# Optimization experiments

Hardware: AMD Instinct MI355X
Metric: run time of the kernel (lower is better)

Reference implementation:

```python
import jax, jax.numpy as jnp
import numpy as np

N, C, D, H, W = 2, 16, 32, 128, 128
CLAMP_MIN, CLAMP_MAX = 1e-8, 1e8


def setup_inputs() -> dict:
    key = jax.random.key(0)
    k1, k2, k3 = jax.random.split(key, 3)
    pred = jax.random.uniform(k1, (N, C, D, H, W), dtype=jnp.float32)
    # target holds the discretized ordinal label, replicated across channel dim
    t = jax.random.randint(k2, (N, 1, D, H, W), 0, C, dtype=jnp.int32)
    target = jnp.broadcast_to(t, (N, C, D, H, W)).astype(jnp.int32)
    mask = jax.random.randint(k3, (N, 1, D, H, W), 0, 2, dtype=jnp.int32)
    return {"pred": pred, "target": target, "mask": mask}


def reference(pred, target, mask):
    n, c, d, h, w = pred.shape
    valid = (mask[:, 0] > 0).reshape(-1)              # [N*D*H*W]
    # channel-first flatten: matches pred.transpose(0,1) then boolean index
    p = jnp.moveaxis(pred, 1, 0).reshape(c, -1)       # [C, M]
    t = jnppos = jnp.moveaxis(target, 1, 0).reshape(c, -1)  # [C, M]
    K = jnp.arange(c, dtype=jnp.int32)[:, None]       # [C, 1]
    m0 = (K <= t) & valid[None, :]                    # ordinal bins below label
    m1 = (K > t) & valid[None, :]                     # ordinal bins above label
    log_p = jnp.log(jnp.clip(p, CLAMP_MIN, CLAMP_MAX))
    log_1mp = jnp.log(jnp.clip(1.0 - p, CLAMP_MIN, CLAMP_MAX))
    s = jnp.sum(jnp.where(m0, log_p, 0.0)) + jnp.sum(jnp.where(m1, log_1mp, 0.0))
    S = jnp.sum(valid).astype(pred.dtype)             # number of masked voxels
    return s / (-S)
```

## Files before the change

kernel.cpp:

```cpp
#include <hip/hip_runtime.h>


constexpr int  kC     = 16;
constexpr int  kDHW   = 32 * 128 * 128;
constexpr long kM     = 2L * kDHW;
constexpr int  kBlock = 256;
constexpr int  kVox   = 4;
constexpr int  kGrid  = (int)(kM / kVox / kBlock);

__global__ __launch_bounds__(kBlock)
void ordloss_main(const float* __restrict__ pred,
                  const int*   __restrict__ target,
                  const int*   __restrict__ mask,
                  float*       __restrict__ bsum,
                  int*         __restrict__ bcnt) {
    const int  tid  = blockIdx.x * kBlock + threadIdx.x;
    const long base = (long)tid * kVox;
    const int  n    = (int)(base >> 19);
    const int  sp   = (int)(base & (kDHW - 1));

    const float* pb = pred + ((size_t)n << 23) + sp;
    float4 p[kC];
    #pragma unroll
    for (int c = 0; c < kC; ++c)
        p[c] = *reinterpret_cast<const float4*>(pb + ((size_t)c << 19));
    const int4 mk = *reinterpret_cast<const int4*>(mask + base);
    const int4 tg = *reinterpret_cast<const int4*>(target + ((size_t)n << 23) + sp);

    float acc0 = 0.f, acc1 = 0.f, acc2 = 0.f, acc3 = 0.f;
    #pragma unroll
    for (int c = 0; c < kC; ++c) {
        float x0 = (c <= tg.x) ? p[c].x : 1.0f - p[c].x;
        float x1 = (c <= tg.y) ? p[c].y : 1.0f - p[c].y;
        float x2 = (c <= tg.z) ? p[c].z : 1.0f - p[c].z;
        float x3 = (c <= tg.w) ? p[c].w : 1.0f - p[c].w;
        acc0 += __logf(fmaxf(x0, 1e-8f));
        acc1 += __logf(fmaxf(x1, 1e-8f));
        acc2 += __logf(fmaxf(x2, 1e-8f));
        acc3 += __logf(fmaxf(x3, 1e-8f));
    }

    float lsum = (mk.x > 0 ? acc0 : 0.f) + (mk.y > 0 ? acc1 : 0.f)
               + (mk.z > 0 ? acc2 : 0.f) + (mk.w > 0 ? acc3 : 0.f);
    int   lcnt = (mk.x > 0) + (mk.y > 0) + (mk.z > 0) + (mk.w > 0);

    #pragma unroll
    for (int off = 32; off > 0; off >>= 1) {
        lsum += __shfl_down(lsum, off);
        lcnt += __shfl_down(lcnt, off);
    }
    __shared__ float swave[kBlock / 64];
    __shared__ int   cwave[kBlock / 64];
    const int lane = threadIdx.x & 63;
    const int wid  = threadIdx.x >> 6;
    if (lane == 0) { swave[wid] = lsum; cwave[wid] = lcnt; }
    __syncthreads();
    if (threadIdx.x == 0) {
        bsum[blockIdx.x] = swave[0] + swave[1] + swave[2] + swave[3];
        bcnt[blockIdx.x] = cwave[0] + cwave[1] + cwave[2] + cwave[3];
    }
}

__global__ __launch_bounds__(kBlock)
void ordloss_reduce(const float* __restrict__ bsum,
                    const int*   __restrict__ bcnt,
                    float*       __restrict__ out) {
    const float4 s4 = *reinterpret_cast<const float4*>(bsum + threadIdx.x * 4);
    const int4   c4 = *reinterpret_cast<const int4*>(bcnt + threadIdx.x * 4);
    double s = (double)s4.x + s4.y + s4.z + s4.w;
    long   c = (long)c4.x + c4.y + c4.z + c4.w;
    #pragma unroll
    for (int off = 32; off > 0; off >>= 1) {
        s += __shfl_down(s, off);
        c += __shfl_down(c, off);
    }
    __shared__ double sw[kBlock / 64];
    __shared__ long   cw[kBlock / 64];
    const int lane = threadIdx.x & 63;
    const int wid  = threadIdx.x >> 6;
    if (lane == 0) { sw[wid] = s; cw[wid] = c; }
    __syncthreads();
    if (threadIdx.x == 0) {
        double S = sw[0] + sw[1] + sw[2] + sw[3];
        long   C = cw[0] + cw[1] + cw[2] + cw[3];
        out[0] = (float)(S / (double)(-C));
    }
}

extern "C" void kernel_launch(void* const* d_in, const int* in_sizes, int n_in,
                              void* d_out, int out_size, void* d_ws, size_t ws_size,
                              hipStream_t stream) {
    const float* pred   = (const float*)d_in[0];
    const int*   target = (const int*)d_in[1];
    const int*   mask   = (const int*)d_in[2];
    float*       bsum   = (float*)d_ws;
    int*         bcnt   = (int*)((char*)d_ws + kGrid * sizeof(float));
    float*       out    = (float*)d_out;

    ordloss_main<<<kGrid, kBlock, 0, stream>>>(pred, target, mask, bsum, bcnt);
    ordloss_reduce<<<1, kBlock, 0, stream>>>(bsum, bcnt, out);
}
```

Before: 137.2 us.

## Parallelize over channels: one float4 per thread, re-reading target and mask

Each thread now processes one float4 of a single channel instead of all 16 channels for 4 voxels, giving 16x more blocks (16384) and fewer registers per thread. Target and mask are re-read per channel, which mostly hits cache since target is contiguous per channel. Masked counts are written only by channel-0 blocks, and the reduce kernel now sums 16384 partial sums. The kernel is memory-bound, so the gain depends on better latency hiding versus extra index traffic and more block-level reductions.

```diff
diff --git a/kernel.cpp b/kernel.cpp
--- a/kernel.cpp
+++ b/kernel.cpp
@@ -1,12 +1,13 @@
 #include <hip/hip_runtime.h>
 
 
-constexpr int  kC     = 16;
-constexpr int  kDHW   = 32 * 128 * 128;
-constexpr long kM     = 2L * kDHW;
-constexpr int  kBlock = 256;
-constexpr int  kVox   = 4;
-constexpr int  kGrid  = (int)(kM / kVox / kBlock);
+constexpr int kC    = 16;
+constexpr int kDHW  = 32 * 128 * 128;
+constexpr int kTot  = 2 * kC * kDHW;
+constexpr int kBlock = 256;
+constexpr int kElem  = kBlock * 4;
+constexpr int kGrid  = kTot / kElem;
+constexpr int kCntBlocks = 2 * (kDHW / kElem);
 
 __global__ __launch_bounds__(kBlock)
 void ordloss_main(const float* __restrict__ pred,
@@ -14,34 +15,23 @@
                   const int*   __restrict__ mask,
                   float*       __restrict__ bsum,
                   int*         __restrict__ bcnt) {
-    const int  tid  = blockIdx.x * kBlock + threadIdx.x;
-    const long base = (long)tid * kVox;
-    const int  n    = (int)(base >> 19);
-    const int  sp   = (int)(base & (kDHW - 1));
+    const int f    = (blockIdx.x * kBlock + threadIdx.x) * 4;
+    const int n    = f >> 23;
+    const int c    = (f >> 19) & 15;
+    const int sp   = f & (kDHW - 1);
 
-    const float* pb = pred + ((size_t)n << 23) + sp;
-    float4 p[kC];
-    #pragma unroll
-    for (int c = 0; c < kC; ++c)
-        p[c] = *reinterpret_cast<const float4*>(pb + ((size_t)c << 19));
-    const int4 mk = *reinterpret_cast<const int4*>(mask + base);
-    const int4 tg = *reinterpret_cast<const int4*>(target + ((size_t)n << 23) + sp);
+    const float4 p  = *reinterpret_cast<const float4*>(pred + f);
+    const int4   tg = *reinterpret_cast<const int4*>(target + ((size_t)n << 23) + sp);
+    const int4   mk = *reinterpret_cast<const int4*>(mask + ((size_t)n << 19) + sp);
 
-    float acc0 = 0.f, acc1 = 0.f, acc2 = 0.f, acc3 = 0.f;
-    #pragma unroll
-    for (int c = 0; c < kC; ++c) {
-        float x0 = (c <= tg.x) ? p[c].x : 1.0f - p[c].x;
-        float x1 = (c <= tg.y) ? p[c].y : 1.0f - p[c].y;
-        float x2 = (c <= tg.z) ? p[c].z : 1.0f - p[c].z;
-        float x3 = (c <= tg.w) ? p[c].w : 1.0f - p[c].w;
-        acc0 += __logf(fmaxf(x0, 1e-8f));
-        acc1 += __logf(fmaxf(x1, 1e-8f));
-        acc2 += __logf(fmaxf(x2, 1e-8f));
-        acc3 += __logf(fmaxf(x3, 1e-8f));
-    }
-
-    float lsum = (mk.x > 0 ? acc0 : 0.f) + (mk.y > 0 ? acc1 : 0.f)
-               + (mk.z > 0 ? acc2 : 0.f) + (mk.w > 0 ? acc3 : 0.f);
+    float x0 = (c <= tg.x) ? p.x : 1.0f - p.x;
+    float x1 = (c <= tg.y) ? p.y : 1.0f - p.y;
+    float x2 = (c <= tg.z) ? p.z : 1.0f - p.z;
+    float x3 = (c <= tg.w) ? p.w : 1.0f - p.w;
+    float lsum = (mk.x > 0 ? __logf(fmaxf(x0, 1e-8f)) : 0.f)
+               + (mk.y > 0 ? __logf(fmaxf(x1, 1e-8f)) : 0.f)
+               + (mk.z > 0 ? __logf(fmaxf(x2, 1e-8f)) : 0.f)
+               + (mk.w > 0 ? __logf(fmaxf(x3, 1e-8f)) : 0.f);
     int   lcnt = (mk.x > 0) + (mk.y > 0) + (mk.z > 0) + (mk.w > 0);
 
     #pragma unroll
@@ -57,7 +47,10 @@
     __syncthreads();
     if (threadIdx.x == 0) {
         bsum[blockIdx.x] = swave[0] + swave[1] + swave[2] + swave[3];
-        bcnt[blockIdx.x] = cwave[0] + cwave[1] + cwave[2] + cwave[3];
+        if (c == 0) {
+            const int sb = sp >> 10;
+            bcnt[(n << 9) + sb] = cwave[0] + cwave[1] + cwave[2] + cwave[3];
+        }
     }
 }
 
@@ -65,10 +58,15 @@
 void ordloss_reduce(const float* __restrict__ bsum,
                     const int*   __restrict__ bcnt,
                     float*       __restrict__ out) {
-    const float4 s4 = *reinterpret_cast<const float4*>(bsum + threadIdx.x * 4);
-    const int4   c4 = *reinterpret_cast<const int4*>(bcnt + threadIdx.x * 4);
-    double s = (double)s4.x + s4.y + s4.z + s4.w;
-    long   c = (long)c4.x + c4.y + c4.z + c4.w;
+    double s = 0.0;
+    #pragma unroll
+    for (int j = 0; j < 16; ++j) {
+        const float4 v = *reinterpret_cast<const float4*>(bsum + (j * kBlock + threadIdx.x) * 4);
+        s += (double)v.x + v.y + v.z + v.w;
+    }
+    const int4 c4 = *reinterpret_cast<const int4*>(bcnt + threadIdx.x * 4);
+    long c = (long)c4.x + c4.y + c4.z + c4.w;
+
     #pragma unroll
     for (int off = 32; off > 0; off >>= 1) {
         s += __shfl_down(s, off);
```

After: 141.6 us. +3.2%, slower.
